# Kernel optimization log

Measured on AMD Instinct MI355X. Metric: run time of the kernel, lower is better.

## Reference

```python
import jax, jax.numpy as jnp
import numpy as np


def setup_inputs() -> dict:
    key = jax.random.key(0)
    k0, k1 = jax.random.split(key)
    b, n, m, e = 8, 2048, 2048, 1024
    mat_0 = jax.random.normal(k0, (b, n, e), dtype=jnp.float32)
    mat_1 = jax.random.normal(k1, (b, m, e), dtype=jnp.float32)
    return {"mat_0": mat_0, "mat_1": mat_1}


def reference(mat_0, mat_1):
    # Original tiles to [b,n,m,e], multiplies, and sums over e.
    # Mathematically identical to a batched QK^T matmul: [b,n,m].
    return jnp.einsum('bne,bme->bnm', mat_0, mat_1)
```

## Files before the change

kernel.cpp:

```cpp
#include <hip/hip_runtime.h>

typedef __attribute__((ext_vector_type(8))) short short8;
typedef __attribute__((ext_vector_type(4))) float f32x4;
typedef __attribute__((ext_vector_type(2))) unsigned int u32x2;
typedef unsigned short u16;

static constexpr int BATCH = 8;
static constexpr int NDIM  = 2048;
static constexpr int MDIM  = 2048;
static constexpr int EDIM  = 1024;
static constexpr int BM    = 128;
static constexpr int BN    = 128;
static constexpr int BK    = 64;

#define BAR() do { asm volatile("" ::: "memory"); \
                   __builtin_amdgcn_s_barrier(); \
                   asm volatile("" ::: "memory"); } while (0)
#define WFENCE() asm volatile("s_waitcnt lgkmcnt(0)" ::: "memory")

__global__ __launch_bounds__(256, 2)
void bmm_fused_kernel(const float* __restrict__ A, const float* __restrict__ B,
                      float* __restrict__ C) {
  __shared__ u16 sh[2][2][BM * BK];

  const int tid  = threadIdx.x;
  const int lane = tid & 63;
  const int wave = tid >> 6;
  const int quad = lane >> 4;
  const int ml   = lane & 15;
  const int wrow = (wave >> 1) * 64;
  const int wcol = (wave & 1) * 64;

  const int flat  = (int)blockIdx.x + 16 * (int)blockIdx.y + 256 * (int)blockIdx.z;
  const int nf    = (flat & 7) * 256 + (flat >> 3);
  const int batch = nf >> 8;
  const int trow  = (nf >> 4) & 15;
  const int tcol  = nf & 15;

  const float* Ab = A + (size_t)batch * NDIM * EDIM + (size_t)trow * BM * EDIM;
  const float* Bb = B + (size_t)batch * MDIM * EDIM + (size_t)tcol * BN * EDIM;

  const int rowb = tid >> 4;
  const int ci   = tid & 15;
  const int colf = ci * 4;
  const int swzoff = (((ci >> 1) ^ (rowb & 7)) << 3) | ((ci & 1) << 2);
  const float* pA = Ab + (size_t)rowb * EDIM + colf;
  const float* pB = Bb + (size_t)rowb * EDIM + colf;

  const int aOff = (wrow + ml) * 64;
  const int bOff = (wcol + ml) * 64;
  const int kc0 = ((quad    ) ^ (ml & 7)) * 8;
  const int kc1 = ((quad + 4) ^ (ml & 7)) * 8;

  short8 ar[2][2], br[4][2];
  f32x4 acc[4][4] = {};
  f32x4 SA0[4], SA1[4], SB0[4], SB1[4];

#define ISS(Sp, P, u, t) do {                                                  \
    const float* _p = (P) + (size_t)((u) * 64) * EDIM + (size_t)(t) * BK;      \
    Sp[0] = *(const f32x4*)(_p);                                               \
    Sp[1] = *(const f32x4*)(_p + (size_t)16 * EDIM);                           \
    Sp[2] = *(const f32x4*)(_p + (size_t)32 * EDIM);                           \
    Sp[3] = *(const f32x4*)(_p + (size_t)48 * EDIM);                           \
  } while (0)

#define WRT(Sp, buf, ab, u) do {                                               \
    _Pragma("unroll")                                                          \
    for (int _j = 0; _j < 4; ++_j) {                                           \
      unsigned _lo, _hi;                                                       \
      asm("v_cvt_pk_bf16_f32 %0, %1, %2"                                       \
          : "=v"(_lo) : "v"(Sp[_j][0]), "v"(Sp[_j][1]));                       \
      asm("v_cvt_pk_bf16_f32 %0, %1, %2"                                       \
          : "=v"(_hi) : "v"(Sp[_j][2]), "v"(Sp[_j][3]));                       \
      u32x2 _u; _u[0] = _lo; _u[1] = _hi;                                      \
      *(u32x2*)&sh[buf][ab][((u) * 64 + rowb + _j * 16) * 64 + swzoff] = _u;   \
    } } while (0)

#define LDA(buf, mh) do {                                                      \
    _Pragma("unroll")                                                          \
    for (int _s = 0; _s < 2; ++_s) {                                           \
      ar[_s][0] = *(const short8*)&sh[buf][0][aOff + ((mh)*32 + _s*16)*64 + kc0];\
      ar[_s][1] = *(const short8*)&sh[buf][0][aOff + ((mh)*32 + _s*16)*64 + kc1];\
    } } while (0)

#define LDBALL(buf) do {                                                       \
    _Pragma("unroll")                                                          \
    for (int _n = 0; _n < 4; ++_n) {                                           \
      br[_n][0] = *(const short8*)&sh[buf][1][bOff + _n*1024 + kc0];           \
      br[_n][1] = *(const short8*)&sh[buf][1][bOff + _n*1024 + kc1];           \
    } } while (0)

#define MM2(mh) do {                                                           \
    __builtin_amdgcn_s_setprio(1);                                             \
    _Pragma("unroll")                                                          \
    for (int _sa = 0; _sa < 2; ++_sa)                                          \
      _Pragma("unroll")                                                        \
      for (int _n = 0; _n < 4; ++_n)                                           \
        _Pragma("unroll")                                                      \
        for (int _ks = 0; _ks < 2; ++_ks)                                      \
          acc[(mh)*2 + _sa][_n] = __builtin_amdgcn_mfma_f32_16x16x32_bf16(     \
              ar[_sa][_ks], br[_n][_ks], acc[(mh)*2 + _sa][_n], 0, 0, 0);      \
    __builtin_amdgcn_s_setprio(0);                                             \
  } while (0)

  ISS(SA0, pA, 0, 0); ISS(SA1, pA, 1, 0); ISS(SB0, pB, 0, 0); ISS(SB1, pB, 1, 0);
  WRT(SA0, 0, 0, 0);  WRT(SA1, 0, 0, 1);  WRT(SB0, 0, 1, 0);  WRT(SB1, 0, 1, 1);
  ISS(SA0, pA, 0, 1); ISS(SA1, pA, 1, 1); ISS(SB0, pB, 0, 1); ISS(SB1, pB, 1, 1);
  WFENCE();
  BAR();

#pragma unroll 1
  for (int u = 0; u < 16; ++u) {
    const int b  = u & 1;
    const int w  = b ^ 1;
    const int tp = (u < 14) ? u + 2 : 15;
    LDA(b, 0); LDBALL(b);
    MM2(0);
    __builtin_amdgcn_sched_barrier(0);
    WRT(SA0, w, 0, 0); WRT(SA1, w, 0, 1);
    ISS(SA0, pA, 0, tp); ISS(SA1, pA, 1, tp);
    WFENCE(); BAR();
    LDA(b, 1);
    MM2(1);
    __builtin_amdgcn_sched_barrier(0);
    WRT(SB0, w, 1, 0); WRT(SB1, w, 1, 1);
    ISS(SB0, pB, 0, tp); ISS(SB1, pB, 1, tp);
    WFENCE(); BAR();
  }

  float* Cb = C + (size_t)batch * NDIM * MDIM
                + (size_t)(trow * BM + wrow + quad * 4) * MDIM
                + (tcol * BN + wcol + ml);
#pragma unroll
  for (int mi = 0; mi < 4; ++mi) {
#pragma unroll
    for (int ni = 0; ni < 4; ++ni) {
      float* cp = Cb + (size_t)(mi * 16) * MDIM + ni * 16;
#pragma unroll
      for (int r = 0; r < 4; ++r)
        cp[(size_t)r * MDIM] = acc[mi][ni][r];
    }
  }
#undef ISS
#undef WRT
#undef LDA
#undef LDBALL
#undef MM2
}

extern "C" void kernel_launch(void* const* d_in, const int* in_sizes, int n_in,
                              void* d_out, int out_size, void* d_ws, size_t ws_size,
                              hipStream_t stream) {
  const float* A = (const float*)d_in[0];
  const float* B = (const float*)d_in[1];
  float*       C = (float*)d_out;
  (void)d_ws; (void)ws_size;

  dim3 grid(MDIM / BN, NDIM / BM, BATCH);
  bmm_fused_kernel<<<grid, dim3(256), 0, stream>>>(A, B, C);
}
```

Before: 317.8 us.

## Restructure main loop to one barrier per K-step with all A fragments preloaded

The loop now loads all four A fragments and all B fragments from shared memory up front, then interleaves the bf16 convert-and-store of the next tile and the global prefetch between two halves of the MFMA work. This halves the barriers per iteration from two to one and skips redundant writes and loads on the final iterations. It also removes the sched_barrier hints, so instruction ordering is left to the compiler. In exchange, register pressure rises because of the extra A fragment registers, which could hurt occupancy under the 2-waves launch bound.

Result: slower. 327.8 us (+3.1%).

```diff
diff --git a/kernel.cpp b/kernel.cpp
--- a/kernel.cpp
+++ b/kernel.cpp
@@ -52,7 +52,7 @@
   const int kc0 = ((quad    ) ^ (ml & 7)) * 8;
   const int kc1 = ((quad + 4) ^ (ml & 7)) * 8;
 
-  short8 ar[2][2], br[4][2];
+  short8 ar[4][2], br[4][2];
   f32x4 acc[4][4] = {};
   f32x4 SA0[4], SA1[4], SB0[4], SB1[4];
 
@@ -76,11 +76,18 @@
       *(u32x2*)&sh[buf][ab][((u) * 64 + rowb + _j * 16) * 64 + swzoff] = _u;   \
     } } while (0)
 
-#define LDA(buf, mh) do {                                                      \
+#define LDA01(buf) do {                                                        \
     _Pragma("unroll")                                                          \
     for (int _s = 0; _s < 2; ++_s) {                                           \
-      ar[_s][0] = *(const short8*)&sh[buf][0][aOff + ((mh)*32 + _s*16)*64 + kc0];\
-      ar[_s][1] = *(const short8*)&sh[buf][0][aOff + ((mh)*32 + _s*16)*64 + kc1];\
+      ar[_s][0] = *(const short8*)&sh[buf][0][aOff + _s*1024 + kc0];           \
+      ar[_s][1] = *(const short8*)&sh[buf][0][aOff + _s*1024 + kc1];           \
+    } } while (0)
+
+#define LDA23(buf) do {                                                        \
+    _Pragma("unroll")                                                          \
+    for (int _s = 2; _s < 4; ++_s) {                                           \
+      ar[_s][0] = *(const short8*)&sh[buf][0][aOff + _s*1024 + kc0];           \
+      ar[_s][1] = *(const short8*)&sh[buf][0][aOff + _s*1024 + kc1];           \
     } } while (0)
 
 #define LDBALL(buf) do {                                                       \
@@ -90,16 +97,16 @@
       br[_n][1] = *(const short8*)&sh[buf][1][bOff + _n*1024 + kc1];           \
     } } while (0)
 
-#define MM2(mh) do {                                                           \
+#define MMH(h) do {                                                            \
     __builtin_amdgcn_s_setprio(1);                                             \
     _Pragma("unroll")                                                          \
-    for (int _sa = 0; _sa < 2; ++_sa)                                          \
+    for (int _sa = (h)*2; _sa < (h)*2 + 2; ++_sa)                              \
       _Pragma("unroll")                                                        \
       for (int _n = 0; _n < 4; ++_n)                                           \
         _Pragma("unroll")                                                      \
         for (int _ks = 0; _ks < 2; ++_ks)                                      \
-          acc[(mh)*2 + _sa][_n] = __builtin_amdgcn_mfma_f32_16x16x32_bf16(     \
-              ar[_sa][_ks], br[_n][_ks], acc[(mh)*2 + _sa][_n], 0, 0, 0);      \
+          acc[_sa][_n] = __builtin_amdgcn_mfma_f32_16x16x32_bf16(              \
+              ar[_sa][_ks], br[_n][_ks], acc[_sa][_n], 0, 0, 0);               \
     __builtin_amdgcn_s_setprio(0);                                             \
   } while (0)
 
@@ -111,20 +118,19 @@
 
 #pragma unroll 1
   for (int u = 0; u < 16; ++u) {
-    const int b  = u & 1;
-    const int w  = b ^ 1;
-    const int tp = (u < 14) ? u + 2 : 15;
-    LDA(b, 0); LDBALL(b);
-    MM2(0);
-    __builtin_amdgcn_sched_barrier(0);
-    WRT(SA0, w, 0, 0); WRT(SA1, w, 0, 1);
-    ISS(SA0, pA, 0, tp); ISS(SA1, pA, 1, tp);
-    WFENCE(); BAR();
-    LDA(b, 1);
-    MM2(1);
-    __builtin_amdgcn_sched_barrier(0);
-    WRT(SB0, w, 1, 0); WRT(SB1, w, 1, 1);
-    ISS(SB0, pB, 0, tp); ISS(SB1, pB, 1, tp);
+    const int b = u & 1;
+    const int w = b ^ 1;
+    LDA01(b); LDBALL(b); LDA23(b);
+    MMH(0);
+    if (u < 15) {
+      WRT(SA0, w, 0, 0); WRT(SA1, w, 0, 1);
+      WRT(SB0, w, 1, 0); WRT(SB1, w, 1, 1);
+    }
+    if (u < 14) {
+      ISS(SA0, pA, 0, u + 2); ISS(SA1, pA, 1, u + 2);
+      ISS(SB0, pB, 0, u + 2); ISS(SB1, pB, 1, u + 2);
+    }
+    MMH(1);
     WFENCE(); BAR();
   }
 
@@ -143,9 +149,10 @@
   }
 #undef ISS
 #undef WRT
-#undef LDA
+#undef LDA01
+#undef LDA23
 #undef LDBALL
-#undef MM2
+#undef MMH
 }
 
 extern "C" void kernel_launch(void* const* d_in, const int* in_sizes, int n_in,
```
